# Performance work log

Hardware: AMD Instinct MI355X
Metric: run time of the kernel (lower is better)

The kernel has to match this reference:

```python
import jax, jax.numpy as jnp
import numpy as np

WS = 7  # window size

def _add_coords(x):
    B, C, H, W = x.shape
    xx = jnp.broadcast_to(jnp.linspace(-1.0, 1.0, W, dtype=x.dtype)[None, None, None, :], (B, 1, H, W))
    yy = jnp.broadcast_to(jnp.linspace(-1.0, 1.0, H, dtype=x.dtype)[None, None, :, None], (B, 1, H, W))
    return jnp.concatenate([x, xx, yy], axis=1)

def setup_inputs() -> dict:
    key = jax.random.key(0)
    k1, k2, k3 = jax.random.split(key, 3)
    in_channels = 62
    inner = in_channels + 2  # 64
    x = jax.random.normal(k1, (8, in_channels, 224, 224), dtype=jnp.float32)
    w_qkv = jax.random.normal(k2, (3 * inner, inner), dtype=jnp.float32) * 0.02
    w_proj = jax.random.normal(k3, (in_channels, inner), dtype=jnp.float32) * 0.02
    b_proj = jnp.zeros((in_channels,), dtype=jnp.float32)
    return {"x": x, "w_qkv": w_qkv, "w_proj": w_proj, "b_proj": b_proj}

def reference(x, w_qkv, w_proj, b_proj):
    xc = _add_coords(x)                       # [B, C, H, W], C = in_channels + 2
    B, C, H, W = xc.shape
    ws = WS
    pad_h = (ws - H % ws) % ws
    pad_w = (ws - W % ws) % ws
    xp = jnp.pad(xc, ((0, 0), (0, 0), (0, pad_h), (0, pad_w)))
    Hp, Wp = xp.shape[2], xp.shape[3]
    nH, nW = Hp // ws, Wp // ws
    # 1x1 conv (no bias) == per-pixel matmul
    qkv = jnp.einsum('oc,bchw->bohw', w_qkv, xp)  # [B, 3C, Hp, Wp]
    # window partition -> [B*nH*nW, 3C, ws*ws]
    qkv = qkv.reshape(B, 3 * C, nH, ws, nW, ws)
    qkv = qkv.transpose(0, 2, 4, 1, 3, 5).reshape(B * nH * nW, 3 * C, ws * ws)
    q, k, v = jnp.split(qkv, 3, axis=1)        # each [Bw, C, ws*ws]
    scale = 1.0 / jnp.sqrt(jnp.asarray(C, dtype=x.dtype))
    attn = jnp.einsum('nci,ncj->nij', q, k) * scale  # [Bw, 49, 49]
    attn = jax.nn.softmax(attn, axis=-1)
    out = jnp.einsum('ncj,nij->nci', v, attn)        # v @ attn^T
    # window merge -> [B, C, Hp, Wp]
    out = out.reshape(B, nH, nW, C, ws, ws).transpose(0, 3, 1, 4, 2, 5).reshape(B, C, Hp, Wp)
    out = out[:, :, :H, :W]
    # 1x1 conv projection with bias, inner -> in_channels
    return jnp.einsum('oc,bchw->bohw', w_proj, out) + b_proj[None, :, None, None]
```

## Files before the change

### kernel.cpp

```cpp
#include <hip/hip_runtime.h>
#include <hip/hip_bf16.h>

typedef __attribute__((ext_vector_type(8))) __bf16 bf16x8;
typedef __attribute__((ext_vector_type(4))) float f32x4;
typedef unsigned short u16;

#define CIN   62
#define HW    224
#define NPIX  49

__device__ __forceinline__ u16 f2b(float f) {
    union { __hip_bfloat16 h; u16 u; } cv;
    cv.h = __float2bfloat16(f);
    return cv.u;
}

__device__ __forceinline__ bf16x8 ld8(const u16* buf, int row, int ecol) {
    int idx = (row << 6) + (ecol ^ ((row & 7) << 3));
    return *reinterpret_cast<const bf16x8*>(buf + idx);
}
__device__ __forceinline__ void st1(u16* buf, int row, int ecol, u16 v) {
    buf[(row << 6) + (ecol ^ ((row & 7) << 3))] = v;
}
__device__ __forceinline__ void st4(u16* buf, int row, int ecol, u16 a, u16 b, u16 c, u16 d) {
    int idx = (row << 6) + (ecol ^ ((row & 7) << 3));
    *reinterpret_cast<ushort4*>(buf + idx) = make_ushort4(a, b, c, d);
}

__global__ void prep_weights(const float* __restrict__ wqkv, const float* __restrict__ wp,
                             u16* __restrict__ wb) {
    int t = blockIdx.x * 256 + threadIdx.x;
    if (t >= 128 * 64) return;
    int o = t >> 6;
    int c = t & 63;
    float s = 0.0f;
    if (o < 64) {
        for (int m = 0; m < 64; ++m)
            s += wqkv[m * 64 + o] * wqkv[(64 + m) * 64 + c];
        s *= 0.125f;
    } else {
        int of = o - 64;
        if (of < CIN)
            for (int m = 0; m < 64; ++m)
                s += wp[of * 64 + m] * wqkv[(128 + m) * 64 + c];
    }
    wb[t] = f2b(s);
}

__global__ __launch_bounds__(256, 6) void win_attn(
    const float* __restrict__ x, const u16* __restrict__ wb,
    const float* __restrict__ bproj, float* __restrict__ out)
{
    __shared__ __align__(16) u16 t0[64 * 64];
    __shared__ __align__(16) u16 t1[64 * 64];
    __shared__ __align__(16) u16 t2[64 * 64];

    const int tid  = threadIdx.x;
    const int lane = tid & 63;
    const int wid  = tid >> 6;
    const int lr   = lane & 15;
    const int lg   = lane >> 4;

    const int win = ((blockIdx.x & 7) << 10) | (blockIdx.x >> 3);
    const int b   = win >> 10;
    const int rem = win & 1023;
    const int hn  = rem >> 5;
    const int wn  = rem & 31;
    const int h0  = hn * 7, w0 = wn * 7;

    {
        const int p = tid & 63;
        const bool valid = p < NPIX;
        const int dh = p / 7, dw = p - dh * 7;
        const int h = h0 + dh, w = w0 + dw;
        const float cx = -1.0f + (2.0f / 223.0f) * (float)w;
        const float cy = -1.0f + (2.0f / 223.0f) * (float)h;
        const float* xp = x + (size_t)b * CIN * HW * HW + (size_t)h * HW + w;
#pragma unroll
        for (int it = 0; it < 16; ++it) {
            int c = (tid >> 6) + it * 4;
            float v = 0.0f;
            if (valid) {
                if (c < CIN)      v = xp[(size_t)c * HW * HW];
                else if (c == 62) v = cx;
                else              v = cy;
            }
            st1(t0, p, c, f2b(v));
        }
    }
    __syncthreads();

    const f32x4 fz = {0.f, 0.f, 0.f, 0.f};

    f32x4 acc[2][4];
#pragma unroll
    for (int m = 0; m < 2; ++m)
#pragma unroll
        for (int n = 0; n < 4; ++n) acc[m][n] = fz;

#pragma unroll
    for (int ks = 0; ks < 2; ++ks) {
        bf16x8 a[2];
#pragma unroll
        for (int m = 0; m < 2; ++m) {
            int o = (wid * 2 + m) * 16 + lr;
            a[m] = *reinterpret_cast<const bf16x8*>(wb + o * 64 + ks * 32 + lg * 8);
        }
#pragma unroll
        for (int n = 0; n < 4; ++n) {
            bf16x8 bb = ld8(t0, n * 16 + lr, ks * 32 + lg * 8);
#pragma unroll
            for (int m = 0; m < 2; ++m)
                acc[m][n] = __builtin_amdgcn_mfma_f32_16x16x32_bf16(a[m], bb, acc[m][n], 0, 0, 0);
        }
    }

#pragma unroll
    for (int m = 0; m < 2; ++m) {
        int mt = wid * 2 + m;
#pragma unroll
        for (int n = 0; n < 4; ++n) {
            int j = n * 16 + lr;
            if (mt < 4) {
                int gb = mt * 16 + lg * 4;
                st4(t1, j, gb, f2b(acc[m][n][0]), f2b(acc[m][n][1]),
                               f2b(acc[m][n][2]), f2b(acc[m][n][3]));
            } else {
                int cb = (mt - 4) * 16 + lg * 4;
#pragma unroll
                for (int r = 0; r < 4; ++r)
                    st1(t2, cb + r, j, f2b(acc[m][n][r]));
            }
        }
    }
    __syncthreads();

    f32x4 s4[4];
#pragma unroll
    for (int n = 0; n < 4; ++n) s4[n] = fz;
#pragma unroll
    for (int ks = 0; ks < 2; ++ks) {
        bf16x8 aq = ld8(t0, wid * 16 + lr, ks * 32 + lg * 8);
#pragma unroll
        for (int n = 0; n < 4; ++n) {
            bf16x8 bt = ld8(t1, n * 16 + lr, ks * 32 + lg * 8);
            s4[n] = __builtin_amdgcn_mfma_f32_16x16x32_bf16(aq, bt, s4[n], 0, 0, 0);
        }
    }

#pragma unroll
    for (int r = 0; r < 4; ++r) {
        const int i = wid * 16 + lg * 4 + r;
        float v[4], mx = -1e30f;
#pragma unroll
        for (int n = 0; n < 4; ++n) {
            v[n] = s4[n][r];
            int j = n * 16 + lr;
            mx = fmaxf(mx, (j < NPIX) ? v[n] : -1e30f);
        }
        mx = fmaxf(mx, __shfl_xor(mx, 1));
        mx = fmaxf(mx, __shfl_xor(mx, 2));
        mx = fmaxf(mx, __shfl_xor(mx, 4));
        mx = fmaxf(mx, __shfl_xor(mx, 8));
        float e[4], sm = 0.f;
#pragma unroll
        for (int n = 0; n < 4; ++n) {
            int j = n * 16 + lr;
            e[n] = (j < NPIX) ? __expf(v[n] - mx) : 0.f;
            sm += e[n];
        }
        sm += __shfl_xor(sm, 1);
        sm += __shfl_xor(sm, 2);
        sm += __shfl_xor(sm, 4);
        sm += __shfl_xor(sm, 8);
        float sinv = 1.0f / sm;
#pragma unroll
        for (int n = 0; n < 4; ++n)
            st1(t0, i, n * 16 + lr, f2b(e[n] * sinv));
    }
    __syncthreads();

    f32x4 y4[4];
#pragma unroll
    for (int n = 0; n < 4; ++n) y4[n] = fz;
#pragma unroll
    for (int ks = 0; ks < 2; ++ks) {
        bf16x8 af = ld8(t2, wid * 16 + lr, ks * 32 + lg * 8);
#pragma unroll
        for (int n = 0; n < 4; ++n) {
            bf16x8 bp = ld8(t0, n * 16 + lr, ks * 32 + lg * 8);
            y4[n] = __builtin_amdgcn_mfma_f32_16x16x32_bf16(af, bp, y4[n], 0, 0, 0);
        }
    }

    const int cb = wid * 16 + lg * 4;
    float bias[4];
#pragma unroll
    for (int r = 0; r < 4; ++r) bias[r] = (cb + r < CIN) ? bproj[cb + r] : 0.f;
#pragma unroll
    for (int n = 0; n < 4; ++n) {
        int p = n * 16 + lr;
        if (p < NPIX) {
            int dh = p / 7, dw = p - dh * 7;
            int h = h0 + dh, w = w0 + dw;
#pragma unroll
            for (int r = 0; r < 4; ++r) {
                int co = cb + r;
                if (co < CIN)
                    out[((b * CIN + co) * HW + h) * HW + w] = y4[n][r] + bias[r];
            }
        }
    }
}

extern "C" void kernel_launch(void* const* d_in, const int* in_sizes, int n_in,
                              void* d_out, int out_size, void* d_ws, size_t ws_size,
                              hipStream_t stream) {
    const float* x    = (const float*)d_in[0];
    const float* wqkv = (const float*)d_in[1];
    const float* wp   = (const float*)d_in[2];
    const float* bp   = (const float*)d_in[3];
    float* out = (float*)d_out;

    u16* wb = (u16*)d_ws;

    prep_weights<<<32, 256, 0, stream>>>(wqkv, wp, wb);
    win_attn<<<8192, 256, 0, stream>>>(x, wb, bp, out);
}
```

Before: 95.77 us.

## Keep input tile in registers as MFMA operand, drop t0 shared buffer

Each wave now loads its own 16 pixels of x straight into bf16 MFMA fragments instead of staging the whole window in a shared-memory tile. The first matmul is split per pixel tile, with each wave computing all 128 output rows for its pixels, and the same fragments are reused as the Q operand for the score matmul. Dropping the third LDS buffer cuts shared memory per block and a sync, so launch bounds rise to 8 blocks per CU. The trade is more weight loads per wave and less coalesced global reads of x, since each lane now gathers 16 channel values.

```diff
diff --git a/kernel.cpp b/kernel.cpp
--- a/kernel.cpp
+++ b/kernel.cpp
@@ -47,11 +47,10 @@
     wb[t] = f2b(s);
 }
 
-__global__ __launch_bounds__(256, 6) void win_attn(
+__global__ __launch_bounds__(256, 8) void win_attn(
     const float* __restrict__ x, const u16* __restrict__ wb,
     const float* __restrict__ bproj, float* __restrict__ out)
 {
-    __shared__ __align__(16) u16 t0[64 * 64];
     __shared__ __align__(16) u16 t1[64 * 64];
     __shared__ __align__(16) u16 t2[64 * 64];
 
@@ -68,85 +67,75 @@
     const int wn  = rem & 31;
     const int h0  = hn * 7, w0 = wn * 7;
 
+    const int p     = wid * 16 + lr;
+    const bool valid = p < NPIX;
+    const int dh = p / 7, dw = p - dh * 7;
+    const int h = h0 + dh, w = w0 + dw;
+    const float cx = -1.0f + (2.0f / 223.0f) * (float)w;
+    const float cy = -1.0f + (2.0f / 223.0f) * (float)h;
+    const float* xp = x + (size_t)b * CIN * HW * HW + (size_t)h * HW + w;
+
+    union { bf16x8 v; u16 u[8]; } xa[2];
+#pragma unroll
+    for (int ks = 0; ks < 2; ++ks)
+#pragma unroll
+        for (int e = 0; e < 8; ++e) {
+            int c = ks * 32 + lg * 8 + e;
+            float v = 0.0f;
+            if (valid)
+                v = (c < CIN) ? xp[(size_t)c * HW * HW] : ((c == 62) ? cx : cy);
+            xa[ks].u[e] = f2b(v);
+        }
+
+    const f32x4 fz = {0.f, 0.f, 0.f, 0.f};
+
     {
-        const int p = tid & 63;
-        const bool valid = p < NPIX;
-        const int dh = p / 7, dw = p - dh * 7;
-        const int h = h0 + dh, w = w0 + dw;
-        const float cx = -1.0f + (2.0f / 223.0f) * (float)w;
-        const float cy = -1.0f + (2.0f / 223.0f) * (float)h;
-        const float* xp = x + (size_t)b * CIN * HW * HW + (size_t)h * HW + w;
-#pragma unroll
-        for (int it = 0; it < 16; ++it) {
-            int c = (tid >> 6) + it * 4;
-            float v = 0.0f;
-            if (valid) {
-                if (c < CIN)      v = xp[(size_t)c * HW * HW];
-                else if (c == 62) v = cx;
-                else              v = cy;
+        f32x4 acc1[4];
+#pragma unroll
+        for (int m = 0; m < 4; ++m) acc1[m] = fz;
+#pragma unroll
+        for (int ks = 0; ks < 2; ++ks)
+#pragma unroll
+            for (int m = 0; m < 4; ++m) {
+                bf16x8 a = *reinterpret_cast<const bf16x8*>(wb + (m * 16 + lr) * 64 + ks * 32 + lg * 8);
+                acc1[m] = __builtin_amdgcn_mfma_f32_16x16x32_bf16(a, xa[ks].v, acc1[m], 0, 0, 0);
             }
-            st1(t0, p, c, f2b(v));
-        }
+#pragma unroll
+        for (int m = 0; m < 4; ++m)
+            st4(t1, p, m * 16 + lg * 4, f2b(acc1[m][0]), f2b(acc1[m][1]),
+                                        f2b(acc1[m][2]), f2b(acc1[m][3]));
+    }
+
+    {
+        f32x4 acc1[4];
+#pragma unroll
+        for (int m = 0; m < 4; ++m) acc1[m] = fz;
+#pragma unroll
+        for (int ks = 0; ks < 2; ++ks)
+#pragma unroll
+            for (int m = 0; m < 4; ++m) {
+                bf16x8 a = *reinterpret_cast<const bf16x8*>(wb + ((m + 4) * 16 + lr) * 64 + ks * 32 + lg * 8);
+                acc1[m] = __builtin_amdgcn_mfma_f32_16x16x32_bf16(a, xa[ks].v, acc1[m], 0, 0, 0);
+            }
+#pragma unroll
+        for (int m = 0; m < 4; ++m)
+#pragma unroll
+            for (int r = 0; r < 4; ++r)
+                st1(t2, m * 16 + lg * 4 + r, p, f2b(acc1[m][r]));
     }
     __syncthreads();
 
-    const f32x4 fz = {0.f, 0.f, 0.f, 0.f};
-
-    f32x4 acc[2][4];
-#pragma unroll
-    for (int m = 0; m < 2; ++m)
-#pragma unroll
-        for (int n = 0; n < 4; ++n) acc[m][n] = fz;
-
-#pragma unroll
-    for (int ks = 0; ks < 2; ++ks) {
-        bf16x8 a[2];
-#pragma unroll
-        for (int m = 0; m < 2; ++m) {
-            int o = (wid * 2 + m) * 16 + lr;
-            a[m] = *reinterpret_cast<const bf16x8*>(wb + o * 64 + ks * 32 + lg * 8);
-        }
-#pragma unroll
-        for (int n = 0; n < 4; ++n) {
-            bf16x8 bb = ld8(t0, n * 16 + lr, ks * 32 + lg * 8);
-#pragma unroll
-            for (int m = 0; m < 2; ++m)
-                acc[m][n] = __builtin_amdgcn_mfma_f32_16x16x32_bf16(a[m], bb, acc[m][n], 0, 0, 0);
-        }
-    }
-
-#pragma unroll
-    for (int m = 0; m < 2; ++m) {
-        int mt = wid * 2 + m;
-#pragma unroll
-        for (int n = 0; n < 4; ++n) {
-            int j = n * 16 + lr;
-            if (mt < 4) {
-                int gb = mt * 16 + lg * 4;
-                st4(t1, j, gb, f2b(acc[m][n][0]), f2b(acc[m][n][1]),
-                               f2b(acc[m][n][2]), f2b(acc[m][n][3]));
-            } else {
-                int cb = (mt - 4) * 16 + lg * 4;
-#pragma unroll
-                for (int r = 0; r < 4; ++r)
-                    st1(t2, cb + r, j, f2b(acc[m][n][r]));
-            }
-        }
-    }
+    f32x4 s4[4];
+#pragma unroll
+    for (int n = 0; n < 4; ++n) s4[n] = fz;
+#pragma unroll
+    for (int ks = 0; ks < 2; ++ks)
+#pragma unroll
+        for (int n = 0; n < 4; ++n) {
+            bf16x8 bt = ld8(t1, n * 16 + lr, ks * 32 + lg * 8);
+            s4[n] = __builtin_amdgcn_mfma_f32_16x16x32_bf16(xa[ks].v, bt, s4[n], 0, 0, 0);
+        }
     __syncthreads();
-
-    f32x4 s4[4];
-#pragma unroll
-    for (int n = 0; n < 4; ++n) s4[n] = fz;
-#pragma unroll
-    for (int ks = 0; ks < 2; ++ks) {
-        bf16x8 aq = ld8(t0, wid * 16 + lr, ks * 32 + lg * 8);
-#pragma unroll
-        for (int n = 0; n < 4; ++n) {
-            bf16x8 bt = ld8(t1, n * 16 + lr, ks * 32 + lg * 8);
-            s4[n] = __builtin_amdgcn_mfma_f32_16x16x32_bf16(aq, bt, s4[n], 0, 0, 0);
-        }
-    }
 
 #pragma unroll
     for (int r = 0; r < 4; ++r) {
@@ -176,7 +165,7 @@
         float sinv = 1.0f / sm;
 #pragma unroll
         for (int n = 0; n < 4; ++n)
-            st1(t0, i, n * 16 + lr, f2b(e[n] * sinv));
+            st1(t1, i, n * 16 + lr, f2b(e[n] * sinv));
     }
     __syncthreads();
 
@@ -188,7 +177,7 @@
         bf16x8 af = ld8(t2, wid * 16 + lr, ks * 32 + lg * 8);
 #pragma unroll
         for (int n = 0; n < 4; ++n) {
-            bf16x8 bp = ld8(t0, n * 16 + lr, ks * 32 + lg * 8);
+            bf16x8 bp = ld8(t1, n * 16 + lr, ks * 32 + lg * 8);
             y4[n] = __builtin_amdgcn_mfma_f32_16x16x32_bf16(af, bp, y4[n], 0, 0, 0);
         }
     }
@@ -199,15 +188,15 @@
     for (int r = 0; r < 4; ++r) bias[r] = (cb + r < CIN) ? bproj[cb + r] : 0.f;
 #pragma unroll
     for (int n = 0; n < 4; ++n) {
-        int p = n * 16 + lr;
-        if (p < NPIX) {
-            int dh = p / 7, dw = p - dh * 7;
-            int h = h0 + dh, w = w0 + dw;
+        int po = n * 16 + lr;
+        if (po < NPIX) {
+            int dho = po / 7, dwo = po - dho * 7;
+            int ho = h0 + dho, wo = w0 + dwo;
 #pragma unroll
             for (int r = 0; r < 4; ++r) {
                 int co = cb + r;
                 if (co < CIN)
-                    out[((b * CIN + co) * HW + h) * HW + w] = y4[n][r] + bias[r];
+                    out[((b * CIN + co) * HW + ho) * HW + wo] = y4[n][r] + bias[r];
             }
         }
     }
```

Result: slower. 122.0 us (+27.4%).

## Process four windows per block with double-buffered input prefetch

Applied to the files above, without the earlier changes.

Each block now handles four consecutive windows of one batch image. It prefetches the next window's input into registers while computing the current one, then writes them into a second LDS buffer. Weight fragments and bias are loaded once per block into registers instead of once per window. The softmax max-subtraction is dropped, relying on small scores to avoid exp overflow; this saves shuffles but risks overflow for other inputs.

```diff
diff --git a/kernel.cpp b/kernel.cpp
--- a/kernel.cpp
+++ b/kernel.cpp
@@ -8,6 +8,7 @@
 #define CIN   62
 #define HW    224
 #define NPIX  49
+#define NWIN  4
 
 __device__ __forceinline__ u16 f2b(float f) {
     union { __hip_bfloat16 h; u16 u; } cv;
@@ -47,13 +48,13 @@
     wb[t] = f2b(s);
 }
 
-__global__ __launch_bounds__(256, 6) void win_attn(
+__global__ __launch_bounds__(256, 5) void win_attn(
     const float* __restrict__ x, const u16* __restrict__ wb,
     const float* __restrict__ bproj, float* __restrict__ out)
 {
-    __shared__ __align__(16) u16 t0[64 * 64];
-    __shared__ __align__(16) u16 t1[64 * 64];
-    __shared__ __align__(16) u16 t2[64 * 64];
+    __shared__ __align__(16) u16 tX[2][64 * 64];
+    __shared__ __align__(16) u16 tT[64 * 64];
+    __shared__ __align__(16) u16 tF[64 * 64];
 
     const int tid  = threadIdx.x;
     const int lane = tid & 63;
@@ -61,155 +62,183 @@
     const int lr   = lane & 15;
     const int lg   = lane >> 4;
 
-    const int win = ((blockIdx.x & 7) << 10) | (blockIdx.x >> 3);
-    const int b   = win >> 10;
-    const int rem = win & 1023;
-    const int hn  = rem >> 5;
-    const int wn  = rem & 31;
-    const int h0  = hn * 7, w0 = wn * 7;
+    const int bid      = blockIdx.x;
+    const int b        = bid & 7;
+    const int win_base = (bid >> 3) << 2;
+
+    const size_t plane = (size_t)HW * HW;
+    const float* xb = x + (size_t)b * CIN * plane;
+    float* ob = out + (size_t)b * CIN * plane;
+
+    const int sp  = tid & 63;
+    const int scq = tid >> 6;
+    const bool svalid = sp < NPIX;
+    const int sdh = sp / 7, sdw = sp - sdh * 7;
+
+    bf16x8 wa[2][2];
+#pragma unroll
+    for (int m = 0; m < 2; ++m)
+#pragma unroll
+        for (int ks = 0; ks < 2; ++ks)
+            wa[m][ks] = *reinterpret_cast<const bf16x8*>(
+                wb + ((wid * 2 + m) * 16 + lr) * 64 + ks * 32 + lg * 8);
+    const int cb = wid * 16 + lg * 4;
+    float bias[4];
+#pragma unroll
+    for (int r = 0; r < 4; ++r) bias[r] = (cb + r < CIN) ? bproj[cb + r] : 0.f;
+
+    const f32x4 fz = {0.f, 0.f, 0.f, 0.f};
 
     {
-        const int p = tid & 63;
-        const bool valid = p < NPIX;
-        const int dh = p / 7, dw = p - dh * 7;
-        const int h = h0 + dh, w = w0 + dw;
+        const int rem = win_base;
+        const int h = (rem >> 5) * 7 + sdh, w = (rem & 31) * 7 + sdw;
         const float cx = -1.0f + (2.0f / 223.0f) * (float)w;
         const float cy = -1.0f + (2.0f / 223.0f) * (float)h;
-        const float* xp = x + (size_t)b * CIN * HW * HW + (size_t)h * HW + w;
+        const float* xp = xb + (size_t)h * HW + w;
 #pragma unroll
         for (int it = 0; it < 16; ++it) {
-            int c = (tid >> 6) + it * 4;
+            int c = scq + it * 4;
             float v = 0.0f;
-            if (valid) {
-                if (c < CIN)      v = xp[(size_t)c * HW * HW];
+            if (svalid) {
+                if (c < CIN)      v = xp[(size_t)c * plane];
                 else if (c == 62) v = cx;
                 else              v = cy;
             }
-            st1(t0, p, c, f2b(v));
+            st1(tX[0], sp, c, f2b(v));
         }
     }
     __syncthreads();
 
-    const f32x4 fz = {0.f, 0.f, 0.f, 0.f};
-
-    f32x4 acc[2][4];
-#pragma unroll
-    for (int m = 0; m < 2; ++m)
-#pragma unroll
-        for (int n = 0; n < 4; ++n) acc[m][n] = fz;
-
-#pragma unroll
-    for (int ks = 0; ks < 2; ++ks) {
-        bf16x8 a[2];
-#pragma unroll
-        for (int m = 0; m < 2; ++m) {
-            int o = (wid * 2 + m) * 16 + lr;
-            a[m] = *reinterpret_cast<const bf16x8*>(wb + o * 64 + ks * 32 + lg * 8);
+#pragma unroll
+    for (int i = 0; i < NWIN; ++i) {
+        const int win = win_base + i;
+        const int h0 = (win >> 5) * 7, w0 = (win & 31) * 7;
+        u16* cur = tX[i & 1];
+        u16* nxt = tX[(i + 1) & 1];
+
+        float xv[16];
+        if (i < NWIN - 1) {
+            const int nwin = win + 1;
+            const int nh = (nwin >> 5) * 7 + sdh, nw = (nwin & 31) * 7 + sdw;
+            const float ncx = -1.0f + (2.0f / 223.0f) * (float)nw;
+            const float ncy = -1.0f + (2.0f / 223.0f) * (float)nh;
+            const float* nxp = xb + (size_t)nh * HW + nw;
+#pragma unroll
+            for (int it = 0; it < 16; ++it) {
+                int c = scq + it * 4;
+                float v = 0.0f;
+                if (svalid) {
+                    if (c < CIN)      v = nxp[(size_t)c * plane];
+                    else if (c == 62) v = ncx;
+                    else              v = ncy;
+                }
+                xv[it] = v;
+            }
+        }
+
+        {
+            f32x4 acc[2][4];
+#pragma unroll
+            for (int m = 0; m < 2; ++m)
+#pragma unroll
+                for (int n = 0; n < 4; ++n) acc[m][n] = fz;
+#pragma unroll
+            for (int ks = 0; ks < 2; ++ks)
+#pragma unroll
+                for (int n = 0; n < 4; ++n) {
+                    bf16x8 bb = ld8(cur, n * 16 + lr, ks * 32 + lg * 8);
+#pragma unroll
+                    for (int m = 0; m < 2; ++m)
+                        acc[m][n] = __builtin_amdgcn_mfma_f32_16x16x32_bf16(wa[m][ks], bb, acc[m][n], 0, 0, 0);
+                }
+#pragma unroll
+            for (int m = 0; m < 2; ++m) {
+                int mt = wid * 2 + m;
+#pragma unroll
+                for (int n = 0; n < 4; ++n) {
+                    int j = n * 16 + lr;
+                    if (mt < 4) {
+                        st4(tT, j, mt * 16 + lg * 4,
+                            f2b(acc[m][n][0]), f2b(acc[m][n][1]),
+                            f2b(acc[m][n][2]), f2b(acc[m][n][3]));
+                    } else {
+                        int cb2 = (mt - 4) * 16 + lg * 4;
+#pragma unroll
+                        for (int r = 0; r < 4; ++r)
+                            st1(tF, cb2 + r, j, f2b(acc[m][n][r]));
+                    }
+                }
+            }
+        }
+        __syncthreads();
+
+        f32x4 s4[4];
+#pragma unroll
+        for (int n = 0; n < 4; ++n) s4[n] = fz;
+#pragma unroll
+        for (int ks = 0; ks < 2; ++ks) {
+            bf16x8 aq = ld8(cur, wid * 16 + lr, ks * 32 + lg * 8);
+#pragma unroll
+            for (int n = 0; n < 4; ++n) {
+                bf16x8 bt = ld8(tT, n * 16 + lr, ks * 32 + lg * 8);
+                s4[n] = __builtin_amdgcn_mfma_f32_16x16x32_bf16(aq, bt, s4[n], 0, 0, 0);
+            }
+        }
+
+#pragma unroll
+        for (int r = 0; r < 4; ++r) {
+            const int irow = wid * 16 + lg * 4 + r;
+            float e[4], sm = 0.f;
+#pragma unroll
+            for (int n = 0; n < 4; ++n) {
+                int j = n * 16 + lr;
+                e[n] = (j < NPIX) ? __expf(s4[n][r]) : 0.f;
+                sm += e[n];
+            }
+            sm += __shfl_xor(sm, 1);
+            sm += __shfl_xor(sm, 2);
+            sm += __shfl_xor(sm, 4);
+            sm += __shfl_xor(sm, 8);
+            float sinv = 1.0f / sm;
+#pragma unroll
+            for (int n = 0; n < 4; ++n)
+                st1(cur, irow, n * 16 + lr, f2b(e[n] * sinv));
+        }
+        __syncthreads();
+
+        f32x4 y4[4];
+#pragma unroll
+        for (int n = 0; n < 4; ++n) y4[n] = fz;
+#pragma unroll
+        for (int ks = 0; ks < 2; ++ks) {
+            bf16x8 af = ld8(tF, wid * 16 + lr, ks * 32 + lg * 8);
+#pragma unroll
+            for (int n = 0; n < 4; ++n) {
+                bf16x8 bp = ld8(cur, n * 16 + lr, ks * 32 + lg * 8);
+                y4[n] = __builtin_amdgcn_mfma_f32_16x16x32_bf16(af, bp, y4[n], 0, 0, 0);
+            }
         }
 #pragma unroll
         for (int n = 0; n < 4; ++n) {
-            bf16x8 bb = ld8(t0, n * 16 + lr, ks * 32 + lg * 8);
-#pragma unroll
-            for (int m = 0; m < 2; ++m)
-                acc[m][n] = __builtin_amdgcn_mfma_f32_16x16x32_bf16(a[m], bb, acc[m][n], 0, 0, 0);
-        }
-    }
-
-#pragma unroll
-    for (int m = 0; m < 2; ++m) {
-        int mt = wid * 2 + m;
-#pragma unroll
-        for (int n = 0; n < 4; ++n) {
-            int j = n * 16 + lr;
-            if (mt < 4) {
-                int gb = mt * 16 + lg * 4;
-                st4(t1, j, gb, f2b(acc[m][n][0]), f2b(acc[m][n][1]),
-                               f2b(acc[m][n][2]), f2b(acc[m][n][3]));
-            } else {
-                int cb = (mt - 4) * 16 + lg * 4;
-#pragma unroll
-                for (int r = 0; r < 4; ++r)
-                    st1(t2, cb + r, j, f2b(acc[m][n][r]));
-            }
-        }
-    }
-    __syncthreads();
-
-    f32x4 s4[4];
-#pragma unroll
-    for (int n = 0; n < 4; ++n) s4[n] = fz;
-#pragma unroll
-    for (int ks = 0; ks < 2; ++ks) {
-        bf16x8 aq = ld8(t0, wid * 16 + lr, ks * 32 + lg * 8);
-#pragma unroll
-        for (int n = 0; n < 4; ++n) {
-            bf16x8 bt = ld8(t1, n * 16 + lr, ks * 32 + lg * 8);
-            s4[n] = __builtin_amdgcn_mfma_f32_16x16x32_bf16(aq, bt, s4[n], 0, 0, 0);
-        }
-    }
-
-#pragma unroll
-    for (int r = 0; r < 4; ++r) {
-        const int i = wid * 16 + lg * 4 + r;
-        float v[4], mx = -1e30f;
-#pragma unroll
-        for (int n = 0; n < 4; ++n) {
-            v[n] = s4[n][r];
-            int j = n * 16 + lr;
-            mx = fmaxf(mx, (j < NPIX) ? v[n] : -1e30f);
-        }
-        mx = fmaxf(mx, __shfl_xor(mx, 1));
-        mx = fmaxf(mx, __shfl_xor(mx, 2));
-        mx = fmaxf(mx, __shfl_xor(mx, 4));
-        mx = fmaxf(mx, __shfl_xor(mx, 8));
-        float e[4], sm = 0.f;
-#pragma unroll
-        for (int n = 0; n < 4; ++n) {
-            int j = n * 16 + lr;
-            e[n] = (j < NPIX) ? __expf(v[n] - mx) : 0.f;
-            sm += e[n];
-        }
-        sm += __shfl_xor(sm, 1);
-        sm += __shfl_xor(sm, 2);
-        sm += __shfl_xor(sm, 4);
-        sm += __shfl_xor(sm, 8);
-        float sinv = 1.0f / sm;
-#pragma unroll
-        for (int n = 0; n < 4; ++n)
-            st1(t0, i, n * 16 + lr, f2b(e[n] * sinv));
-    }
-    __syncthreads();
-
-    f32x4 y4[4];
-#pragma unroll
-    for (int n = 0; n < 4; ++n) y4[n] = fz;
-#pragma unroll
-    for (int ks = 0; ks < 2; ++ks) {
-        bf16x8 af = ld8(t2, wid * 16 + lr, ks * 32 + lg * 8);
-#pragma unroll
-        for (int n = 0; n < 4; ++n) {
-            bf16x8 bp = ld8(t0, n * 16 + lr, ks * 32 + lg * 8);
-            y4[n] = __builtin_amdgcn_mfma_f32_16x16x32_bf16(af, bp, y4[n], 0, 0, 0);
-        }
-    }
-
-    const int cb = wid * 16 + lg * 4;
-    float bias[4];
-#pragma unroll
-    for (int r = 0; r < 4; ++r) bias[r] = (cb + r < CIN) ? bproj[cb + r] : 0.f;
-#pragma unroll
-    for (int n = 0; n < 4; ++n) {
-        int p = n * 16 + lr;
-        if (p < NPIX) {
-            int dh = p / 7, dw = p - dh * 7;
-            int h = h0 + dh, w = w0 + dw;
-#pragma unroll
-            for (int r = 0; r < 4; ++r) {
-                int co = cb + r;
-                if (co < CIN)
-                    out[((b * CIN + co) * HW + h) * HW + w] = y4[n][r] + bias[r];
-            }
-        }
+            int po = n * 16 + lr;
+            if (po < NPIX) {
+                int dho = po / 7, dwo = po - dho * 7;
+                int ho = h0 + dho, wo = w0 + dwo;
+#pragma unroll
+                for (int r = 0; r < 4; ++r) {
+                    int co = cb + r;
+                    if (co < CIN)
+                        ob[(size_t)co * plane + (size_t)ho * HW + wo] = y4[n][r] + bias[r];
+                }
+            }
+        }
+
+        if (i < NWIN - 1) {
+#pragma unroll
+            for (int it = 0; it < 16; ++it)
+                st1(nxt, sp, scq + it * 4, f2b(xv[it]));
+        }
+        __syncthreads();
     }
 }
 
@@ -225,5 +254,5 @@
     u16* wb = (u16*)d_ws;
 
     prep_weights<<<32, 256, 0, stream>>>(wqkv, wp, wb);
-    win_attn<<<8192, 256, 0, stream>>>(x, wb, bp, out);
-}
+    win_attn<<<2048, 256, 0, stream>>>(x, wb, bp, out);
+}
```

Result: slower. 244.1 us (+154.9%).
